# Kernel optimization log

Measured on AMD Instinct MI355X. Metric: run time of the kernel, lower is better.

Reference implementation:

```python
import jax, jax.numpy as jnp
import numpy as np

B, C, N = 8, 256, 2048
NMOD = 5  # time, space, time_cor, space_cor, global_res


def _attn(x, y, Wqk, Vw, Vb, Tw, Tb):
    """Offset self-attention (PCT-style). x, y: [B, C, N].
    q/k share the same 1x1-conv weight Wqk; v and trans convs have bias.
    softmax over last axis, then L1 renorm over axis=1 of the [B,N,N] map.
    """
    x_q = jnp.einsum('oc,bcn->bno', Wqk, y)           # [B,N,C]
    x_k = jnp.einsum('oc,bcn->bon', Wqk, x)           # [B,C,N]
    x_v = jnp.einsum('oc,bcn->bon', Vw, x) + Vb[:, None]
    att = jax.nn.softmax(jnp.einsum('bnc,bcm->bnm', x_q, x_k), axis=-1)
    att = att / (1e-07 + att.sum(axis=1, keepdims=True))
    x_r = jnp.einsum('bcn,bnm->bcm', x_v, att)        # [B,C,N]
    x_r = jax.nn.relu(jnp.einsum('oc,bcn->bon', Tw, x - x_r) + Tb[:, None])
    return x + x_r


def setup_inputs() -> dict:
    key = jax.random.key(0)
    ks = jax.random.split(key, 6)
    s = 1.0 / np.sqrt(C)
    return {
        'x':   jax.random.normal(ks[0], (B, 3, C, N), dtype=jnp.float32),
        'Wqk': jax.random.normal(ks[1], (NMOD, C, C), dtype=jnp.float32) * s,
        'Vw':  jax.random.normal(ks[2], (NMOD, C, C), dtype=jnp.float32) * s,
        'Vb':  jax.random.normal(ks[3], (NMOD, C), dtype=jnp.float32) * s,
        'Tw':  jax.random.normal(ks[4], (NMOD, C, C), dtype=jnp.float32) * s,
        'Tb':  jax.random.normal(ks[5], (NMOD, C), dtype=jnp.float32) * s,
    }


def reference(x, Wqk, Vw, Vb, Tw, Tb):
    time_x, mid, space_x = x[:, 0], x[:, 1], x[:, 2]

    def A(i, xx, yy):
        return _attn(xx, yy, Wqk[i], Vw[i], Vb[i], Tw[i], Tb[i])

    time_att = A(0, time_x, time_x)
    space_att = A(1, space_x, space_x)
    time_cor = A(2, time_x, space_x)
    space_cor = A(3, space_x, time_x)
    global_feat = A(4, mid, mid)

    time_update = jnp.tanh(time_att * jax.nn.sigmoid(time_cor))
    space_update = jnp.tanh(space_att * jax.nn.sigmoid(space_cor))
    g_sig = jax.nn.sigmoid(global_feat)
    global_residual = jax.nn.sigmoid(time_update * g_sig + space_update * g_sig)
    return mid + global_residual * jnp.tanh(global_feat)
```

## Files before the change

kernel.cpp:

```cpp
#include <hip/hip_runtime.h>
#include <math.h>

#define BB 8
#define CC 256
#define NN 2048

static const size_t NC  = (size_t)NN * CC;
static const size_t CN  = (size_t)CC * NN;

typedef unsigned short u16;
typedef __attribute__((ext_vector_type(8))) short short8;
typedef __attribute__((ext_vector_type(4))) float f32x4;

__device__ __forceinline__ float bf2f(u16 v) {
    union { unsigned int u; float f; } t; t.u = ((unsigned int)v) << 16; return t.f;
}
__device__ __forceinline__ u16 f2bf(float f) {
    union { float f; unsigned int u; } t; t.f = f;
    return (u16)((t.u + 0x7fffu + ((t.u >> 16) & 1u)) >> 16);
}
__device__ __forceinline__ float sigf(float x) { return 1.0f / (1.0f + expf(-x)); }

__device__ __forceinline__ size_t til(int r, int c, int tpr) {
    return (((size_t)((r >> 4) * tpr + (c >> 5))) << 9)
         + (size_t)((r & 15) << 5) + (size_t)(c & 31);
}

__device__ __forceinline__ void stage_tile(const u16* gtile, u16* ldst, int lane) {
    const u16* src = gtile + (lane & 15) * 32 + (lane >> 4) * 8;
    __builtin_amdgcn_global_load_lds(
        (const __attribute__((address_space(1))) void*)src,
        (__attribute__((address_space(3))) void*)ldst, 16, 0, 0);
}
#define WAITV(n) asm volatile("s_waitcnt vmcnt(" #n ")" ::: "memory")

__global__ __launch_bounds__(256) void cast_w(const float* __restrict__ in,
                                              u16* __restrict__ outp)
{
    const int mat = blockIdx.y;
    const int idx = blockIdx.x * 256 + threadIdx.x;
    const int c = idx >> 6, k = (idx & 63) << 2;
    const float4 v = *(const float4*)&in[(size_t)mat * (CC * CC) + (size_t)c * CC + k];
    ushort4 p;
    p.x = f2bf(v.x); p.y = f2bf(v.y); p.z = f2bf(v.z); p.w = f2bf(v.w);
    *(ushort4*)&outp[(size_t)mat * (CC * CC) + til(c, k, CC / 32)] = p;
}

__global__ __launch_bounds__(256) void tcast_x(const float* __restrict__ in,
                                               u16* __restrict__ out)
{
    const int z = blockIdx.z;
    const float* I = in + (size_t)z * CN;
    u16* O = out + (size_t)z * NC;
    const int c0 = blockIdx.y * 64, n0 = blockIdx.x * 64;
    const int tx = threadIdx.x & 15, ty = threadIdx.x >> 4;

    __shared__ float t[64][68];

    #pragma unroll
    for (int cc = 0; cc < 64; cc += 16) {
        const int c = ty + cc;
        *(float4*)&t[c][tx * 4] = *(const float4*)&I[(size_t)(c0 + c) * NN + n0 + tx * 4];
    }
    __syncthreads();
    #pragma unroll
    for (int nn2 = 0; nn2 < 64; nn2 += 16) {
        const int n = n0 + ty + nn2;
        const int c = c0 + tx * 4;
        ushort4 p;
        p.x = f2bf(t[tx * 4 + 0][ty + nn2]);
        p.y = f2bf(t[tx * 4 + 1][ty + nn2]);
        p.z = f2bf(t[tx * 4 + 2][ty + nn2]);
        p.w = f2bf(t[tx * 4 + 3][ty + nn2]);
        *(ushort4*)&O[til(n, c, 8)] = p;
    }
}

struct QkvP {
    const u16* w[12]; const u16* x[12]; u16* out[12];
    const float* bias[12]; int isv[12];
};

__global__ __launch_bounds__(256) void conv_qkv(QkvP P)
{
    const int z = blockIdx.z, job = z >> 3, b = z & 7;
    const int isv = P.isv[job];
    const u16* Wp = P.w[job];
    const u16* Xp = P.x[job] + (size_t)b * (3 * NC);
    const int n0 = blockIdx.x * 128, c0 = blockIdx.y * 128;
    const int lane = threadIdx.x & 63, wave = threadIdx.x >> 6;
    const int l15 = lane & 15, lg = lane >> 4;
    const int rA = (wave >> 1) * 64, rB = (wave & 1) * 64;

    const u16* Ab = isv ? Xp : Wp;
    const u16* Bb = isv ? Wp : Xp;
    const int Ar0 = (isv ? n0 : c0) + rA;
    const int Br0 = (isv ? c0 : n0) + rB;

    __shared__ u16 ring[4][16][512];
    u16* rw = &ring[wave][0][0];

    auto stage8 = [&](int kc, int grp) {
        #pragma unroll
        for (int i = 0; i < 4; i++)
            stage_tile(Ab + ((size_t)((Ar0 >> 4) + i) * 8 + kc) * 512,
                       rw + (size_t)(grp + i) * 512, lane);
        #pragma unroll
        for (int i = 0; i < 4; i++)
            stage_tile(Bb + ((size_t)((Br0 >> 4) + i) * 8 + kc) * 512,
                       rw + (size_t)(grp + 4 + i) * 512, lane);
    };

    stage8(0, 0);
    stage8(1, 8);

    const int roff = lg * 128 + l15 * 8;
    f32x4 acc[4][4] = {};

    #pragma unroll
    for (int kc = 0; kc < 8; kc++) {
        if (kc < 7) { WAITV(8); } else { WAITV(0); }
        const int g = (kc & 1) * 8;
        short8 av[4], bv[4];
        #pragma unroll
        for (int i = 0; i < 4; i++) av[i] = *(const short8*)&rw[(size_t)(g + i) * 512 + roff];
        #pragma unroll
        for (int i = 0; i < 4; i++) bv[i] = *(const short8*)&rw[(size_t)(g + 4 + i) * 512 + roff];
        asm volatile("s_waitcnt lgkmcnt(0)" ::: "memory");
        __builtin_amdgcn_sched_barrier(0);
        if (kc + 2 < 8) stage8(kc + 2, g);
        __builtin_amdgcn_s_setprio(1);
        #pragma unroll
        for (int i = 0; i < 4; i++)
            #pragma unroll
            for (int j = 0; j < 4; j++)
                acc[i][j] = __builtin_amdgcn_mfma_f32_16x16x32_bf16(av[i], bv[j], acc[i][j], 0, 0, 0);
        __builtin_amdgcn_s_setprio(0);
    }

    if (!isv) {
        u16* Ot = P.out[job] + (size_t)b * NC;
        #pragma unroll
        for (int i = 0; i < 4; i++) {
            const int c = c0 + rA + i * 16 + lg * 4;
            #pragma unroll
            for (int j = 0; j < 4; j++) {
                const int n = n0 + rB + j * 16 + l15;
                ushort4 p;
                p.x = f2bf(acc[i][j][0]); p.y = f2bf(acc[i][j][1]);
                p.z = f2bf(acc[i][j][2]); p.w = f2bf(acc[i][j][3]);
                *(ushort4*)&Ot[til(n, c, 8)] = p;
            }
        }
    } else {
        u16* Ov = P.out[job] + (size_t)b * CN;
        const float* bias = P.bias[job];
        #pragma unroll
        for (int j = 0; j < 4; j++) {
            const int c = c0 + rB + j * 16 + l15;
            const float bi = bias[c];
            #pragma unroll
            for (int i = 0; i < 4; i++) {
                const int n = n0 + rA + i * 16 + lg * 4;
                ushort4 p;
                p.x = f2bf(acc[i][j][0] + bi); p.y = f2bf(acc[i][j][1] + bi);
                p.z = f2bf(acc[i][j][2] + bi); p.w = f2bf(acc[i][j][3] + bi);
                *(ushort4*)&Ov[til(c, n, 64)] = p;
            }
        }
    }
}

__global__ __launch_bounds__(256) void conv_t2(
    const u16* __restrict__ W, const u16* __restrict__ Dt,
    const float* __restrict__ bias, const u16* __restrict__ Xts,
    u16* __restrict__ O)
{
    const int bid = blockIdx.x;
    const int b = bid & 7;
    const int rest = bid >> 3;
    const int cy = rest & 1, nx = rest >> 1;
    const int n0 = nx * 128, c0 = cy * 128;
    const int lane = threadIdx.x & 63, wave = threadIdx.x >> 6;
    const int l15 = lane & 15, lg = lane >> 4;
    const int wc = (wave >> 1) * 64, wn = (wave & 1) * 64;

    const u16* Xp = Dt + (size_t)b * NC;
    const u16* ap[4]; const u16* bp[4];
    #pragma unroll
    for (int i = 0; i < 4; i++) {
        ap[i] = W  + til(c0 + wc + i * 16 + l15, lg * 8, 8);
        bp[i] = Xp + til(n0 + wn + i * 16 + l15, lg * 8, 8);
    }

    f32x4 acc[4][4] = {};
    #pragma unroll 2
    for (int kc = 0; kc < 8; kc++) {
        short8 av[4], bv[4];
        #pragma unroll
        for (int i = 0; i < 4; i++) av[i] = *(const short8*)(ap[i] + kc * 512);
        #pragma unroll
        for (int i = 0; i < 4; i++) bv[i] = *(const short8*)(bp[i] + kc * 512);
        #pragma unroll
        for (int i = 0; i < 4; i++)
            #pragma unroll
            for (int j = 0; j < 4; j++)
                acc[i][j] = __builtin_amdgcn_mfma_f32_16x16x32_bf16(av[i], bv[j], acc[i][j], 0, 0, 0);
    }

    const u16* Xtb = Xts + (size_t)b * (3 * NC);
    u16* Ob = O + (size_t)b * CN;
    #pragma unroll
    for (int i = 0; i < 4; i++) {
        const int cb = c0 + wc + i * 16 + lg * 4;
        #pragma unroll
        for (int j = 0; j < 4; j++) {
            const int n = n0 + wn + j * 16 + l15;
            const ushort4 xv = *(const ushort4*)&Xtb[til(n, cb, 8)];
            const u16 xa[4] = { xv.x, xv.y, xv.z, xv.w };
            #pragma unroll
            for (int r = 0; r < 4; r++) {
                const int c = cb + r;
                const float v = bf2f(xa[r]) + fmaxf(acc[i][j][r] + bias[c], 0.0f);
                Ob[til(c, n, 64)] = f2bf(v);
            }
        }
    }
}

__global__ __launch_bounds__(1024) void attn_mfma6(
    const u16* __restrict__ Q, const u16* __restrict__ K,
    u16* __restrict__ Sout, float* __restrict__ CPb)
{
    const int bid = blockIdx.x;
    const int b = bid & 7;
    const int nblk = bid >> 3;
    const int n0 = nblk * 32;
    const int tid = threadIdx.x, lane = tid & 63, wave = tid >> 6;
    const int l15 = lane & 15, lg = lane >> 4;

    const u16* Qt = Q + (size_t)b * NC;
    const u16* Kt = K + (size_t)b * NC;

    __shared__ u16 KL[16 * 8 * 512];
    __shared__ u16 QL[16 * 512];
    __shared__ float red[16][32];
    __shared__ float rowstat[32];

    stage_tile(Qt + ((size_t)((n0 >> 4) + (wave >> 3)) * 8 + (wave & 7)) * 512,
               &QL[wave * 512], lane);
    u16* kw = &KL[wave * 4096];
    #pragma unroll
    for (int p = 0; p < 6; p++)
        stage_tile(Kt + ((size_t)(wave * 8 + (p & 7)) * 8 + (p >> 3)) * 512,
                   &kw[p * 512], lane);
    __syncthreads();

    f32x4 acc[2][8];
    #pragma unroll
    for (int g = 0; g < 2; g++)
        #pragma unroll
        for (int t = 0; t < 8; t++) acc[g][t] = (f32x4){0.f, 0.f, 0.f, 0.f};

    const int roff = lg * 128 + l15 * 8;

    #pragma unroll
    for (int kc = 0; kc < 8; kc++) {
        const short8 a0 = *(const short8*)&QL[kc * 512 + roff];
        const short8 a1 = *(const short8*)&QL[(8 + kc) * 512 + roff];
        #pragma unroll
        for (int t = 0; t < 8; t++) {
            const int i = kc * 8 + t;
            if (i < 58) { WAITV(5); } else if (i == 58) { WAITV(0); }
            const short8 bf = *(const short8*)&kw[(i & 7) * 512 + roff];
            if (i + 6 < 64) {
                const int j = i + 6;
                stage_tile(Kt + ((size_t)(wave * 8 + (j & 7)) * 8 + (j >> 3)) * 512,
                           &kw[(j & 7) * 512], lane);
            }
            __builtin_amdgcn_s_setprio(1);
            acc[0][t] = __builtin_amdgcn_mfma_f32_16x16x32_bf16(a0, bf, acc[0][t], 0, 0, 0);
            acc[1][t] = __builtin_amdgcn_mfma_f32_16x16x32_bf16(a1, bf, acc[1][t], 0, 0, 0);
            __builtin_amdgcn_s_setprio(0);
        }
    }

    float pm[2][4];
    #pragma unroll
    for (int g = 0; g < 2; g++)
        #pragma unroll
        for (int r = 0; r < 4; r++) {
            float m = acc[g][0][r];
            #pragma unroll
            for (int t = 1; t < 8; t++) m = fmaxf(m, acc[g][t][r]);
            #pragma unroll
            for (int o = 1; o <= 8; o <<= 1) m = fmaxf(m, __shfl_xor(m, o));
            pm[g][r] = m;
        }
    if (l15 == 0) {
        #pragma unroll
        for (int g = 0; g < 2; g++)
            #pragma unroll
            for (int r = 0; r < 4; r++) red[wave][g * 16 + lg * 4 + r] = pm[g][r];
    }
    __syncthreads();
    if (tid < 32) {
        float m = red[0][tid];
        #pragma unroll
        for (int w = 1; w < 16; w++) m = fmaxf(m, red[w][tid]);
        rowstat[tid] = m;
    }
    __syncthreads();

    float rm[2][4], ps[2][4];
    #pragma unroll
    for (int g = 0; g < 2; g++)
        #pragma unroll
        for (int r = 0; r < 4; r++) { rm[g][r] = rowstat[g * 16 + lg * 4 + r]; ps[g][r] = 0.f; }
    __syncthreads();

    #pragma unroll
    for (int g = 0; g < 2; g++)
        #pragma unroll
        for (int t = 0; t < 8; t++)
            #pragma unroll
            for (int r = 0; r < 4; r++) {
                const float e = __expf(acc[g][t][r] - rm[g][r]);
                acc[g][t][r] = e; ps[g][r] += e;
            }
    #pragma unroll
    for (int g = 0; g < 2; g++)
        #pragma unroll
        for (int r = 0; r < 4; r++)
            #pragma unroll
            for (int o = 1; o <= 8; o <<= 1) ps[g][r] += __shfl_xor(ps[g][r], o);
    if (l15 == 0) {
        #pragma unroll
        for (int g = 0; g < 2; g++)
            #pragma unroll
            for (int r = 0; r < 4; r++) red[wave][g * 16 + lg * 4 + r] = ps[g][r];
    }
    __syncthreads();
    if (tid < 32) {
        float s = red[0][tid];
        #pragma unroll
        for (int w = 1; w < 16; w++) s += red[w][tid];
        rowstat[tid] = 1.0f / s;
    }
    __syncthreads();

    float rv[2][4];
    #pragma unroll
    for (int g = 0; g < 2; g++)
        #pragma unroll
        for (int r = 0; r < 4; r++) rv[g][r] = rowstat[g * 16 + lg * 4 + r];

    u16* sb = Sout + (size_t)b * NN * NN;
    u16* sbg[2];
    #pragma unroll
    for (int g = 0; g < 2; g++)
        sbg[g] = sb + (size_t)((n0 >> 3) + g * 2 + (lg >> 1)) * (NN * 8) + (lg & 1) * 4;
    float* cpb = CPb + ((size_t)b * 64 + nblk) * NN;

    #pragma unroll
    for (int t = 0; t < 8; t++) {
        const int m = wave * 128 + t * 16 + l15;
        float cs = 0.0f;
        #pragma unroll
        for (int g = 0; g < 2; g++) {
            const float v0 = acc[g][t][0] * rv[g][0], v1 = acc[g][t][1] * rv[g][1];
            const float v2 = acc[g][t][2] * rv[g][2], v3 = acc[g][t][3] * rv[g][3];
            ushort4 pk;
            pk.x = f2bf(v0); pk.y = f2bf(v1); pk.z = f2bf(v2); pk.w = f2bf(v3);
            *(ushort4*)&sbg[g][(size_t)m * 8] = pk;
            cs += v0 + v1 + v2 + v3;
        }
        cs += __shfl_xor(cs, 16);
        cs += __shfl_xor(cs, 32);
        if (lane < 16) cpb[m] = cs;
    }
}

__global__ __launch_bounds__(256) void csum_kernel(const float* __restrict__ cp,
                                                   float* __restrict__ cs)
{
    const int b  = blockIdx.y;
    const int ml = threadIdx.x & 63;
    const int m  = blockIdx.x * 64 + ml;
    const int g0 = threadIdx.x >> 6;
    float s = 0.0f;
    for (int g = g0; g < 64; g += 4)
        s += cp[((size_t)b * 64 + g) * NN + m];
    __shared__ float red[4][64];
    red[g0][ml] = s;
    __syncthreads();
    if (threadIdx.x < 64) {
        cs[(size_t)b * NN + blockIdx.x * 64 + threadIdx.x] =
            red[0][threadIdx.x] + red[1][threadIdx.x] +
            red[2][threadIdx.x] + red[3][threadIdx.x];
    }
}

__global__ __launch_bounds__(256) void pv_mfma(
    const u16* __restrict__ V, const u16* __restrict__ S,
    const float* __restrict__ CSb, const u16* __restrict__ Xts,
    u16* __restrict__ DTo)
{
    const int bid = blockIdx.x;
    const int b = bid & 7;
    const int r2 = bid >> 3;
    const int cy = r2 & 1, mx = r2 >> 1;
    const int m0b = mx * 64, c0 = cy * 128;
    const int lane = threadIdx.x & 63, wave = threadIdx.x >> 6;
    const int wc = (wave >> 1) * 64, wm = (wave & 1) * 32;
    const int l15 = lane & 15, lg = lane >> 4;

    const u16* Vm = V + (size_t)b * CN;
    const u16* Sm = S + (size_t)b * NN * NN;

    f32x4 acc[4][2] = {};
    const u16* vp[4]; const u16* sp[2];
    #pragma unroll
    for (int ai = 0; ai < 4; ai++)
        vp[ai] = Vm + til(c0 + wc + ai * 16 + l15, lg * 8, 64);
    #pragma unroll
    for (int bj = 0; bj < 2; bj++)
        sp[bj] = Sm + ((size_t)lg * NN + m0b + wm + bj * 16 + l15) * 8;

    #pragma unroll 2
    for (int kc = 0; kc < 64; kc++) {
        short8 a[4], s2[2];
        #pragma unroll
        for (int ai = 0; ai < 4; ai++) { a[ai] = *(const short8*)vp[ai]; vp[ai] += 512; }
        #pragma unroll
        for (int bj = 0; bj < 2; bj++) { s2[bj] = *(const short8*)sp[bj]; sp[bj] += (size_t)4 * NN * 8; }
        #pragma unroll
        for (int ai = 0; ai < 4; ai++)
            #pragma unroll
            for (int bj = 0; bj < 2; bj++)
                acc[ai][bj] = __builtin_amdgcn_mfma_f32_16x16x32_bf16(a[ai], s2[bj], acc[ai][bj], 0, 0, 0);
    }

    const u16* Xtb = Xts + (size_t)b * (3 * NC);
    u16* Dtb = DTo + (size_t)b * NC;

    #pragma unroll
    for (int bj = 0; bj < 2; bj++) {
        const int m = m0b + wm + bj * 16 + l15;
        const float inv = 1.0f / (1e-7f + CSb[(size_t)b * NN + m]);
        #pragma unroll
        for (int ai = 0; ai < 4; ai++) {
            const int c = c0 + wc + ai * 16 + lg * 4;
            const size_t ad = til(m, c, 8);
            const ushort4 xv = *(const ushort4*)&Xtb[ad];
            ushort4 pk;
            pk.x = f2bf(bf2f(xv.x) - acc[ai][bj][0] * inv);
            pk.y = f2bf(bf2f(xv.y) - acc[ai][bj][1] * inv);
            pk.z = f2bf(bf2f(xv.z) - acc[ai][bj][2] * inv);
            pk.w = f2bf(bf2f(xv.w) - acc[ai][bj][3] * inv);
            *(ushort4*)&Dtb[ad] = pk;
        }
    }
}

__global__ __launch_bounds__(256) void ew_update_t(u16* __restrict__ A,
                                                   const u16* __restrict__ Bv)
{
    const size_t e = ((size_t)blockIdx.x * 256 + threadIdx.x) * 8;
    short8 a = *(const short8*)&A[e];
    const short8 b = *(const short8*)&Bv[e];
    #pragma unroll
    for (int j = 0; j < 8; j++) {
        const float f = tanhf(bf2f((u16)a[j]) * sigf(bf2f((u16)b[j])));
        a[j] = (short)f2bf(f);
    }
    *(short8*)&A[e] = a;
}

__global__ __launch_bounds__(256) void ew_final_t(
    const u16* __restrict__ TU, const u16* __restrict__ SU,
    const u16* __restrict__ G, const float* __restrict__ x,
    float* __restrict__ OUT)
{
    const size_t e = ((size_t)blockIdx.x * 256 + threadIdx.x) * 8;
    const int b = (int)(e / CN);
    const size_t r = e - (size_t)b * CN;
    const int tile = (int)(r >> 9), win = (int)(r & 511);
    const int row = win >> 5, col = win & 31;
    const int c = (tile >> 6) * 16 + row;
    const int n = (tile & 63) * 32 + col;

    const size_t lin = ((size_t)b * 3 + 1) * CN + (size_t)c * NN + n;
    const float4 m0 = *(const float4*)&x[lin];
    const float4 m1 = *(const float4*)&x[lin + 4];
    const float mid[8] = { m0.x, m0.y, m0.z, m0.w, m1.x, m1.y, m1.z, m1.w };

    const short8 tu = *(const short8*)&TU[e];
    const short8 su = *(const short8*)&SU[e];
    const short8 g  = *(const short8*)&G[e];

    float o[8];
    #pragma unroll
    for (int j = 0; j < 8; j++) {
        const float gg = bf2f((u16)g[j]);
        o[j] = mid[j] + sigf((bf2f((u16)tu[j]) + bf2f((u16)su[j])) * sigf(gg)) * tanhf(gg);
    }
    float* op = OUT + (size_t)b * CN + (size_t)c * NN + n;
    *(float4*)op       = (float4){o[0], o[1], o[2], o[3]};
    *(float4*)(op + 4) = (float4){o[4], o[5], o[6], o[7]};
}

extern "C" void kernel_launch(void* const* d_in, const int* in_sizes, int n_in,
                              void* d_out, int out_size, void* d_ws, size_t ws_size,
                              hipStream_t stream)
{
    const float* x   = (const float*)d_in[0];
    const float* Wqk = (const float*)d_in[1];
    const float* Vw  = (const float*)d_in[2];
    const float* VbF = (const float*)d_in[3];
    const float* Tw  = (const float*)d_in[4];
    const float* TbF = (const float*)d_in[5];
    float* out = (float*)d_out;

    const int mxs[5] = {0, 2, 0, 2, 1};
    const int mys[5] = {0, 2, 2, 0, 1};
    const int qjob[5] = {0, 1, 5, 6, 4};
    const int q_wi[7] = {0, 1, 2, 3, 4, 2, 3};
    const int q_xi[7] = {0, 2, 0, 2, 1, 2, 0};

    const size_t WSZ     = (size_t)CC * CC;
    const size_t QK_SLAB = (size_t)BB * NC;
    const size_t S_SLAB  = (size_t)BB * NN * NN;
    const size_t CP_SLAB = (size_t)BB * 64 * NN;
    const size_t CS_SLAB = (size_t)BB * NN;
    const size_t O_SLAB  = (size_t)BB * CN;

    const size_t base_b = 15 * WSZ * 2 + (size_t)BB * 3 * NC * 2;
    const size_t modtl  = S_SLAB * 2 + CP_SLAB * 4 + CS_SLAB * 4 + QK_SLAB * 2;
    const size_t margin = 2u << 20;
    const size_t need_1 = base_b + 12 * QK_SLAB * 2 + modtl + 3 * O_SLAB * 2 + margin;
    const size_t need_2 = base_b +  3 * QK_SLAB * 2 + modtl + 3 * O_SLAB * 2 + margin;

    const int tier2 = (ws_size >= need_1) ? 0 : 1;
    if (tier2 && ws_size < need_2) return;

    const int nQK = tier2 ? 2 : 7;
    const int nV  = tier2 ? 1 : 5;

    char* ws = (char*)d_ws;
    size_t off = 0;
    auto alloc = [&](size_t bytes) -> char* {
        char* p = ws + off; off += (bytes + 255) & ~255ULL; return p;
    };

    u16*   W16 = (u16*)  alloc(15 * WSZ * 2);
    u16*   Xt  = (u16*)  alloc((size_t)BB * 3 * NC * 2);
    u16*   QK  = (u16*)  alloc((size_t)nQK * QK_SLAB * 2);
    u16*   VB  = (u16*)  alloc((size_t)nV * QK_SLAB * 2);
    u16*   S   = (u16*)  alloc(S_SLAB * 2);
    float* CP  = (float*)alloc(CP_SLAB * 4);
    float* CS  = (float*)alloc(CS_SLAB * 4);
    u16*   DT  = (u16*)  alloc(QK_SLAB * 2);
    u16*   OB  = (u16*)  alloc(3 * O_SLAB * 2);

    cast_w<<<dim3(64, 5), 256, 0, stream>>>(Wqk, W16);
    cast_w<<<dim3(64, 5), 256, 0, stream>>>(Vw,  W16 + 5 * WSZ);
    cast_w<<<dim3(64, 5), 256, 0, stream>>>(Tw,  W16 + 10 * WSZ);
    tcast_x<<<dim3(NN / 64, CC / 64, BB * 3), 256, 0, stream>>>(x, Xt);

    if (!tier2) {
        QkvP qp{};
        for (int j = 0; j < 7; j++) {
            qp.w[j] = W16 + (size_t)q_wi[j] * WSZ;
            qp.x[j] = Xt + (size_t)q_xi[j] * NC;
            qp.out[j] = QK + (size_t)j * QK_SLAB;
            qp.isv[j] = 0; qp.bias[j] = nullptr;
        }
        for (int i = 0; i < 5; i++) {
            const int j = 7 + i;
            qp.w[j] = W16 + (size_t)(5 + i) * WSZ;
            qp.x[j] = Xt + (size_t)mxs[i] * NC;
            qp.out[j] = VB + (size_t)i * QK_SLAB;
            qp.isv[j] = 1; qp.bias[j] = VbF + (size_t)i * CC;
        }
        conv_qkv<<<dim3(NN / 128, CC / 128, 96), 256, 0, stream>>>(qp);
    }

    auto run_mod = [&](int i, u16* O) {
        const u16* Qp; const u16* Kp; const u16* Vp;
        if (!tier2) {
            Qp = QK + (size_t)qjob[i] * QK_SLAB;
            Kp = QK + (size_t)i * QK_SLAB;
            Vp = VB + (size_t)i * QK_SLAB;
        } else {
            QkvP qp{}; int nj = 0;
            qp.w[nj] = W16 + (size_t)i * WSZ; qp.x[nj] = Xt + (size_t)mxs[i] * NC;
            qp.out[nj] = QK; qp.isv[nj] = 0; nj++;
            Qp = QK; Kp = QK;
            if (mys[i] != mxs[i]) {
                qp.w[nj] = W16 + (size_t)i * WSZ; qp.x[nj] = Xt + (size_t)mys[i] * NC;
                qp.out[nj] = QK + QK_SLAB; qp.isv[nj] = 0; nj++;
                Qp = QK + QK_SLAB;
            }
            qp.w[nj] = W16 + (size_t)(5 + i) * WSZ; qp.x[nj] = Xt + (size_t)mxs[i] * NC;
            qp.out[nj] = VB; qp.isv[nj] = 1; qp.bias[nj] = VbF + (size_t)i * CC; nj++;
            conv_qkv<<<dim3(NN / 128, CC / 128, 8 * nj), 256, 0, stream>>>(qp);
            Vp = VB;
        }
        attn_mfma6<<<512, 1024, 0, stream>>>(Qp, Kp, S, CP);
        csum_kernel<<<dim3(NN / 64, BB), 256, 0, stream>>>(CP, CS);
        pv_mfma<<<512, 256, 0, stream>>>(Vp, S, CS, Xt + (size_t)mxs[i] * NC, DT);
        conv_t2<<<256, 256, 0, stream>>>(W16 + (size_t)(10 + i) * WSZ, DT,
                                         TbF + (size_t)i * CC,
                                         Xt + (size_t)mxs[i] * NC, O);
    };

    u16* OB0 = OB;
    u16* OB1 = OB + O_SLAB;
    u16* OB2 = OB + 2 * O_SLAB;
    const int ewg = (int)(((size_t)BB * CN) / (256 * 8));

    run_mod(0, OB0);
    run_mod(2, OB1);
    ew_update_t<<<ewg, 256, 0, stream>>>(OB0, OB1);
    run_mod(1, OB1);
    run_mod(3, OB2);
    ew_update_t<<<ewg, 256, 0, stream>>>(OB1, OB2);
    run_mod(4, OB2);
    ew_final_t<<<ewg, 256, 0, stream>>>(OB0, OB1, OB2, x, out);
}
```

Before: 643.2 us.

## Fuse gating epilogues into trans-conv and widen attention row tile to 64

The separate elementwise update and final kernels are removed. Their tanh/sigmoid gating and the final output computation now run in the conv_t2 epilogue, selected by a template mode, which saves launches and a round trip over the intermediate buffers. The attention kernel now handles 64 query rows per block instead of 32, with a 7-slot, 5-deep K pipeline in LDS and half as many column-sum partials. Each K tile fetched is therefore reused across twice as many rows, in exchange for more accumulator registers and fewer blocks (256). The final mode writes fp32 output with scattered, uncoalesced per-element stores.

```diff
diff --git a/kernel.cpp b/kernel.cpp
--- a/kernel.cpp
+++ b/kernel.cpp
@@ -171,10 +171,12 @@
     }
 }
 
+template<int MODE>
 __global__ __launch_bounds__(256) void conv_t2(
     const u16* __restrict__ W, const u16* __restrict__ Dt,
     const float* __restrict__ bias, const u16* __restrict__ Xts,
-    u16* __restrict__ O)
+    u16* __restrict__ O, const u16* __restrict__ TU,
+    const float* __restrict__ xfull, float* __restrict__ OUT)
 {
     const int bid = blockIdx.x;
     const int b = bid & 7;
@@ -210,6 +212,8 @@
 
     const u16* Xtb = Xts + (size_t)b * (3 * NC);
     u16* Ob = O + (size_t)b * CN;
+    const u16* TUb = (MODE == 2) ? (TU + (size_t)b * CN) : nullptr;
+
     #pragma unroll
     for (int i = 0; i < 4; i++) {
         const int cb = c0 + wc + i * 16 + lg * 4;
@@ -222,43 +226,59 @@
             for (int r = 0; r < 4; r++) {
                 const int c = cb + r;
                 const float v = bf2f(xa[r]) + fmaxf(acc[i][j][r] + bias[c], 0.0f);
-                Ob[til(c, n, 64)] = f2bf(v);
+                const size_t ad = til(c, n, 64);
+                if (MODE == 0) {
+                    Ob[ad] = f2bf(v);
+                } else if (MODE == 1) {
+                    const float a_ = bf2f(Ob[ad]);
+                    Ob[ad] = f2bf(tanhf(a_ * sigf(v)));
+                } else {
+                    const float tu = bf2f(TUb[ad]);
+                    const float su = bf2f(Ob[ad]);
+                    const float mid = xfull[((size_t)b * 3 + 1) * CN + (size_t)c * NN + n];
+                    OUT[(size_t)b * CN + (size_t)c * NN + n] =
+                        mid + sigf((tu + su) * sigf(v)) * tanhf(v);
+                }
             }
         }
     }
 }
 
-__global__ __launch_bounds__(1024) void attn_mfma6(
+__global__ __launch_bounds__(1024) void attn_mfma7(
     const u16* __restrict__ Q, const u16* __restrict__ K,
     u16* __restrict__ Sout, float* __restrict__ CPb)
 {
     const int bid = blockIdx.x;
     const int b = bid & 7;
     const int nblk = bid >> 3;
-    const int n0 = nblk * 32;
+    const int n0 = nblk * 64;
     const int tid = threadIdx.x, lane = tid & 63, wave = tid >> 6;
     const int l15 = lane & 15, lg = lane >> 4;
 
     const u16* Qt = Q + (size_t)b * NC;
     const u16* Kt = K + (size_t)b * NC;
 
-    __shared__ u16 KL[16 * 8 * 512];
-    __shared__ u16 QL[16 * 512];
-    __shared__ float red[16][32];
-    __shared__ float rowstat[32];
-
-    stage_tile(Qt + ((size_t)((n0 >> 4) + (wave >> 3)) * 8 + (wave & 7)) * 512,
-               &QL[wave * 512], lane);
-    u16* kw = &KL[wave * 4096];
-    #pragma unroll
-    for (int p = 0; p < 6; p++)
+    __shared__ u16 KL[16 * 7 * 512];
+    __shared__ u16 QL[32 * 512];
+    __shared__ float red[16][64];
+    __shared__ float rowstat[64];
+
+    #pragma unroll
+    for (int j = 0; j < 2; j++) {
+        const int q = wave * 2 + j;
+        stage_tile(Qt + ((size_t)((n0 >> 4) + (q >> 3)) * 8 + (q & 7)) * 512,
+                   &QL[q * 512], lane);
+    }
+    u16* kw = &KL[wave * 3584];
+    #pragma unroll
+    for (int p = 0; p < 5; p++)
         stage_tile(Kt + ((size_t)(wave * 8 + (p & 7)) * 8 + (p >> 3)) * 512,
                    &kw[p * 512], lane);
     __syncthreads();
 
-    f32x4 acc[2][8];
-    #pragma unroll
-    for (int g = 0; g < 2; g++)
+    f32x4 acc[4][8];
+    #pragma unroll
+    for (int g = 0; g < 4; g++)
         #pragma unroll
         for (int t = 0; t < 8; t++) acc[g][t] = (f32x4){0.f, 0.f, 0.f, 0.f};
 
@@ -266,28 +286,31 @@
 
     #pragma unroll
     for (int kc = 0; kc < 8; kc++) {
-        const short8 a0 = *(const short8*)&QL[kc * 512 + roff];
-        const short8 a1 = *(const short8*)&QL[(8 + kc) * 512 + roff];
+        short8 a[4];
+        #pragma unroll
+        for (int g = 0; g < 4; g++)
+            a[g] = *(const short8*)&QL[(g * 8 + kc) * 512 + roff];
         #pragma unroll
         for (int t = 0; t < 8; t++) {
             const int i = kc * 8 + t;
-            if (i < 58) { WAITV(5); } else if (i == 58) { WAITV(0); }
-            const short8 bf = *(const short8*)&kw[(i & 7) * 512 + roff];
-            if (i + 6 < 64) {
-                const int j = i + 6;
+            if (i < 59) { WAITV(4); } else if (i == 59) { WAITV(0); }
+            const short8 bf = *(const short8*)&kw[(i % 7) * 512 + roff];
+            if (i + 5 < 64) {
+                const int j = i + 5;
                 stage_tile(Kt + ((size_t)(wave * 8 + (j & 7)) * 8 + (j >> 3)) * 512,
-                           &kw[(j & 7) * 512], lane);
+                           &kw[(j % 7) * 512], lane);
             }
             __builtin_amdgcn_s_setprio(1);
-            acc[0][t] = __builtin_amdgcn_mfma_f32_16x16x32_bf16(a0, bf, acc[0][t], 0, 0, 0);
-            acc[1][t] = __builtin_amdgcn_mfma_f32_16x16x32_bf16(a1, bf, acc[1][t], 0, 0, 0);
+            #pragma unroll
+            for (int g = 0; g < 4; g++)
+                acc[g][t] = __builtin_amdgcn_mfma_f32_16x16x32_bf16(a[g], bf, acc[g][t], 0, 0, 0);
             __builtin_amdgcn_s_setprio(0);
         }
     }
 
-    float pm[2][4];
-    #pragma unroll
-    for (int g = 0; g < 2; g++)
+    float pm[4][4];
+    #pragma unroll
+    for (int g = 0; g < 4; g++)
         #pragma unroll
         for (int r = 0; r < 4; r++) {
             float m = acc[g][0][r];
@@ -299,12 +322,12 @@
         }
     if (l15 == 0) {
         #pragma unroll
-        for (int g = 0; g < 2; g++)
+        for (int g = 0; g < 4; g++)
             #pragma unroll
             for (int r = 0; r < 4; r++) red[wave][g * 16 + lg * 4 + r] = pm[g][r];
     }
     __syncthreads();
-    if (tid < 32) {
+    if (tid < 64) {
         float m = red[0][tid];
         #pragma unroll
         for (int w = 1; w < 16; w++) m = fmaxf(m, red[w][tid]);
@@ -312,15 +335,15 @@
     }
     __syncthreads();
 
-    float rm[2][4], ps[2][4];
-    #pragma unroll
-    for (int g = 0; g < 2; g++)
+    float rm[4][4], ps[4][4];
+    #pragma unroll
+    for (int g = 0; g < 4; g++)
         #pragma unroll
         for (int r = 0; r < 4; r++) { rm[g][r] = rowstat[g * 16 + lg * 4 + r]; ps[g][r] = 0.f; }
     __syncthreads();
 
     #pragma unroll
-    for (int g = 0; g < 2; g++)
+    for (int g = 0; g < 4; g++)
         #pragma unroll
         for (int t = 0; t < 8; t++)
             #pragma unroll
@@ -329,19 +352,19 @@
                 acc[g][t][r] = e; ps[g][r] += e;
             }
     #pragma unroll
-    for (int g = 0; g < 2; g++)
+    for (int g = 0; g < 4; g++)
         #pragma unroll
         for (int r = 0; r < 4; r++)
             #pragma unroll
             for (int o = 1; o <= 8; o <<= 1) ps[g][r] += __shfl_xor(ps[g][r], o);
     if (l15 == 0) {
         #pragma unroll
-        for (int g = 0; g < 2; g++)
+        for (int g = 0; g < 4; g++)
             #pragma unroll
             for (int r = 0; r < 4; r++) red[wave][g * 16 + lg * 4 + r] = ps[g][r];
     }
     __syncthreads();
-    if (tid < 32) {
+    if (tid < 64) {
         float s = red[0][tid];
         #pragma unroll
         for (int w = 1; w < 16; w++) s += red[w][tid];
@@ -349,25 +372,25 @@
     }
     __syncthreads();
 
-    float rv[2][4];
-    #pragma unroll
-    for (int g = 0; g < 2; g++)
+    float rv[4][4];
+    #pragma unroll
+    for (int g = 0; g < 4; g++)
         #pragma unroll
         for (int r = 0; r < 4; r++) rv[g][r] = rowstat[g * 16 + lg * 4 + r];
 
     u16* sb = Sout + (size_t)b * NN * NN;
-    u16* sbg[2];
-    #pragma unroll
-    for (int g = 0; g < 2; g++)
+    u16* sbg[4];
+    #pragma unroll
+    for (int g = 0; g < 4; g++)
         sbg[g] = sb + (size_t)((n0 >> 3) + g * 2 + (lg >> 1)) * (NN * 8) + (lg & 1) * 4;
-    float* cpb = CPb + ((size_t)b * 64 + nblk) * NN;
+    float* cpb = CPb + ((size_t)b * 32 + nblk) * NN;
 
     #pragma unroll
     for (int t = 0; t < 8; t++) {
         const int m = wave * 128 + t * 16 + l15;
         float cs = 0.0f;
         #pragma unroll
-        for (int g = 0; g < 2; g++) {
+        for (int g = 0; g < 4; g++) {
             const float v0 = acc[g][t][0] * rv[g][0], v1 = acc[g][t][1] * rv[g][1];
             const float v2 = acc[g][t][2] * rv[g][2], v3 = acc[g][t][3] * rv[g][3];
             ushort4 pk;
@@ -389,8 +412,8 @@
     const int m  = blockIdx.x * 64 + ml;
     const int g0 = threadIdx.x >> 6;
     float s = 0.0f;
-    for (int g = g0; g < 64; g += 4)
-        s += cp[((size_t)b * 64 + g) * NN + m];
+    for (int g = g0; g < 32; g += 4)
+        s += cp[((size_t)b * 32 + g) * NN + m];
     __shared__ float red[4][64];
     red[g0][ml] = s;
     __syncthreads();
@@ -463,53 +486,6 @@
     }
 }
 
-__global__ __launch_bounds__(256) void ew_update_t(u16* __restrict__ A,
-                                                   const u16* __restrict__ Bv)
-{
-    const size_t e = ((size_t)blockIdx.x * 256 + threadIdx.x) * 8;
-    short8 a = *(const short8*)&A[e];
-    const short8 b = *(const short8*)&Bv[e];
-    #pragma unroll
-    for (int j = 0; j < 8; j++) {
-        const float f = tanhf(bf2f((u16)a[j]) * sigf(bf2f((u16)b[j])));
-        a[j] = (short)f2bf(f);
-    }
-    *(short8*)&A[e] = a;
-}
-
-__global__ __launch_bounds__(256) void ew_final_t(
-    const u16* __restrict__ TU, const u16* __restrict__ SU,
-    const u16* __restrict__ G, const float* __restrict__ x,
-    float* __restrict__ OUT)
-{
-    const size_t e = ((size_t)blockIdx.x * 256 + threadIdx.x) * 8;
-    const int b = (int)(e / CN);
-    const size_t r = e - (size_t)b * CN;
-    const int tile = (int)(r >> 9), win = (int)(r & 511);
-    const int row = win >> 5, col = win & 31;
-    const int c = (tile >> 6) * 16 + row;
-    const int n = (tile & 63) * 32 + col;
-
-    const size_t lin = ((size_t)b * 3 + 1) * CN + (size_t)c * NN + n;
-    const float4 m0 = *(const float4*)&x[lin];
-    const float4 m1 = *(const float4*)&x[lin + 4];
-    const float mid[8] = { m0.x, m0.y, m0.z, m0.w, m1.x, m1.y, m1.z, m1.w };
-
-    const short8 tu = *(const short8*)&TU[e];
-    const short8 su = *(const short8*)&SU[e];
-    const short8 g  = *(const short8*)&G[e];
-
-    float o[8];
-    #pragma unroll
-    for (int j = 0; j < 8; j++) {
-        const float gg = bf2f((u16)g[j]);
-        o[j] = mid[j] + sigf((bf2f((u16)tu[j]) + bf2f((u16)su[j])) * sigf(gg)) * tanhf(gg);
-    }
-    float* op = OUT + (size_t)b * CN + (size_t)c * NN + n;
-    *(float4*)op       = (float4){o[0], o[1], o[2], o[3]};
-    *(float4*)(op + 4) = (float4){o[4], o[5], o[6], o[7]};
-}
-
 extern "C" void kernel_launch(void* const* d_in, const int* in_sizes, int n_in,
                               void* d_out, int out_size, void* d_ws, size_t ws_size,
                               hipStream_t stream)
@@ -531,15 +507,15 @@
     const size_t WSZ     = (size_t)CC * CC;
     const size_t QK_SLAB = (size_t)BB * NC;
     const size_t S_SLAB  = (size_t)BB * NN * NN;
-    const size_t CP_SLAB = (size_t)BB * 64 * NN;
+    const size_t CP_SLAB = (size_t)BB * 32 * NN;
     const size_t CS_SLAB = (size_t)BB * NN;
     const size_t O_SLAB  = (size_t)BB * CN;
 
     const size_t base_b = 15 * WSZ * 2 + (size_t)BB * 3 * NC * 2;
     const size_t modtl  = S_SLAB * 2 + CP_SLAB * 4 + CS_SLAB * 4 + QK_SLAB * 2;
     const size_t margin = 2u << 20;
-    const size_t need_1 = base_b + 12 * QK_SLAB * 2 + modtl + 3 * O_SLAB * 2 + margin;
-    const size_t need_2 = base_b +  3 * QK_SLAB * 2 + modtl + 3 * O_SLAB * 2 + margin;
+    const size_t need_1 = base_b + 12 * QK_SLAB * 2 + modtl + 2 * O_SLAB * 2 + margin;
+    const size_t need_2 = base_b +  3 * QK_SLAB * 2 + modtl + 2 * O_SLAB * 2 + margin;
 
     const int tier2 = (ws_size >= need_1) ? 0 : 1;
     if (tier2 && ws_size < need_2) return;
@@ -561,7 +537,7 @@
     float* CP  = (float*)alloc(CP_SLAB * 4);
     float* CS  = (float*)alloc(CS_SLAB * 4);
     u16*   DT  = (u16*)  alloc(QK_SLAB * 2);
-    u16*   OB  = (u16*)  alloc(3 * O_SLAB * 2);
+    u16*   OB  = (u16*)  alloc(2 * O_SLAB * 2);
 
     cast_w<<<dim3(64, 5), 256, 0, stream>>>(Wqk, W16);
     cast_w<<<dim3(64, 5), 256, 0, stream>>>(Vw,  W16 + 5 * WSZ);
@@ -586,7 +562,7 @@
         conv_qkv<<<dim3(NN / 128, CC / 128, 96), 256, 0, stream>>>(qp);
     }
 
-    auto run_mod = [&](int i, u16* O) {
+    auto run_core = [&](int i) {
         const u16* Qp; const u16* Kp; const u16* Vp;
         if (!tier2) {
             Qp = QK + (size_t)qjob[i] * QK_SLAB;
@@ -607,25 +583,32 @@
             conv_qkv<<<dim3(NN / 128, CC / 128, 8 * nj), 256, 0, stream>>>(qp);
             Vp = VB;
         }
-        attn_mfma6<<<512, 1024, 0, stream>>>(Qp, Kp, S, CP);
+        attn_mfma7<<<256, 1024, 0, stream>>>(Qp, Kp, S, CP);
         csum_kernel<<<dim3(NN / 64, BB), 256, 0, stream>>>(CP, CS);
         pv_mfma<<<512, 256, 0, stream>>>(Vp, S, CS, Xt + (size_t)mxs[i] * NC, DT);
-        conv_t2<<<256, 256, 0, stream>>>(W16 + (size_t)(10 + i) * WSZ, DT,
-                                         TbF + (size_t)i * CC,
-                                         Xt + (size_t)mxs[i] * NC, O);
     };
 
     u16* OB0 = OB;
     u16* OB1 = OB + O_SLAB;
-    u16* OB2 = OB + 2 * O_SLAB;
-    const int ewg = (int)(((size_t)BB * CN) / (256 * 8));
-
-    run_mod(0, OB0);
-    run_mod(2, OB1);
-    ew_update_t<<<ewg, 256, 0, stream>>>(OB0, OB1);
-    run_mod(1, OB1);
-    run_mod(3, OB2);
-    ew_update_t<<<ewg, 256, 0, stream>>>(OB1, OB2);
-    run_mod(4, OB2);
-    ew_final_t<<<ewg, 256, 0, stream>>>(OB0, OB1, OB2, x, out);
-}
+
+    run_core(0);
+    conv_t2<0><<<256, 256, 0, stream>>>(W16 + 10 * WSZ, DT, TbF + 0 * CC,
+                                        Xt + (size_t)mxs[0] * NC, OB0,
+                                        nullptr, nullptr, nullptr);
+    run_core(2);
+    conv_t2<1><<<256, 256, 0, stream>>>(W16 + 12 * WSZ, DT, TbF + 2 * CC,
+                                        Xt + (size_t)mxs[2] * NC, OB0,
+                                        nullptr, nullptr, nullptr);
+    run_core(1);
+    conv_t2<0><<<256, 256, 0, stream>>>(W16 + 11 * WSZ, DT, TbF + 1 * CC,
+                                        Xt + (size_t)mxs[1] * NC, OB1,
+                                        nullptr, nullptr, nullptr);
+    run_core(3);
+    conv_t2<1><<<256, 256, 0, stream>>>(W16 + 13 * WSZ, DT, TbF + 3 * CC,
+                                        Xt + (size_t)mxs[3] * NC, OB1,
+                                        nullptr, nullptr, nullptr);
+    run_core(4);
+    conv_t2<2><<<256, 256, 0, stream>>>(W16 + 14 * WSZ, DT, TbF + 4 * CC,
+                                        Xt + (size_t)mxs[4] * NC, OB1,
+                                        OB0, x, out);
+}
```

Measured after the change: 1.434 ms. 2.23x slower.
